# Kernel tuning notes

Hardware: AMD Instinct MI355X
Metric: run time of the kernel (lower is better)

## Reference

```python
import jax, jax.numpy as jnp
import numpy as np

B, L, D_MODEL, D_FF, H = 2, 2048, 512, 512, 8
DK = D_FF // H


def _lin(key, fan_in, fan_out):
    k1, k2 = jax.random.split(key)
    lim = 1.0 / np.sqrt(fan_in)
    W = jax.random.uniform(k1, (fan_in, fan_out), jnp.float32, -lim, lim)
    b = jax.random.uniform(k2, (fan_out,), jnp.float32, -lim, lim)
    return W, b


def setup_inputs() -> dict:
    key = jax.random.key(0)
    ks = jax.random.split(key, 13)
    x = jax.random.normal(ks[0], (B, L, D_MODEL), jnp.float32)
    x_knowledge = jax.random.normal(ks[1], (B, L, D_MODEL), jnp.float32)
    Wv, bv = _lin(ks[2], D_MODEL, D_FF)
    Wk, bk = _lin(ks[3], D_MODEL, D_FF)
    Wq, bq = _lin(ks[4], D_MODEL, D_FF)
    Wkf, bkf = _lin(ks[5], D_MODEL, D_FF)
    Wqf, bqf = _lin(ks[6], D_MODEL, D_FF)
    Wq2, bq2 = _lin(ks[7], D_FF, D_FF)
    Wk2, bk2 = _lin(ks[8], D_FF, D_FF)
    Wkf2, bkf2 = _lin(ks[9], D_FF, D_FF)
    Wqf2, bqf2 = _lin(ks[10], D_FF, D_FF)
    Wo, bo = _lin(ks[11], D_FF, D_MODEL)
    return dict(x=x, x_knowledge=x_knowledge, Wv=Wv, bv=bv, Wk=Wk, bk=bk,
                Wq=Wq, bq=bq, Wkf=Wkf, bkf=bkf, Wqf=Wqf, bqf=bqf,
                Wq2=Wq2, bq2=bq2, Wk2=Wk2, bk2=bk2, Wqf2=Wqf2, bqf2=bqf2,
                Wkf2=Wkf2, bkf2=bkf2, Wo=Wo, bo=bo)


def reference(x, x_knowledge, Wv, bv, Wk, bk, Wq, bq, Wkf, bkf, Wqf, bqf,
              Wq2, bq2, Wk2, bk2, Wqf2, bqf2, Wkf2, bkf2, Wo, bo):
    b, l, _ = x.shape
    # first projections from d_model -> d_ff
    v = x @ Wv + bv
    k = x @ Wk + bk
    q = x @ Wq + bq
    k_fei = x_knowledge @ Wkf + bkf
    q_fei = x_knowledge @ Wqf + bqf
    # second projections + NONSTANDARD head split: raw reshape (B,L,d_ff)->(B,h,L,dk)
    q = (q @ Wq2 + bq2).reshape(b, H, l, DK)
    k = (k @ Wk2 + bk2).reshape(b, H, l, DK)
    q_fei = (q_fei @ Wqf2 + bqf2).reshape(b, H, l, DK)
    k_fei = (k_fei @ Wkf2 + bkf2).reshape(b, H, l, DK)
    scale = 1.0 / np.sqrt(2.0 * DK).astype(np.float32)
    att = jnp.einsum('bhld,bhmd->bhlm', q, k) * scale
    att_fei = jnp.einsum('bhld,bhmd->bhlm', q_fei, k_fei) * scale
    score = jax.nn.softmax(att + att_fei, axis=-1)  # dropout is identity at eval
    v = v.reshape(b, H, l, DK)
    out = jnp.einsum('bhlm,bhmd->bhld', score, v).reshape(b, l, D_FF)
    return out @ Wo + bo
```

## Files before the change

### kernel.cpp

```cpp
#include <hip/hip_runtime.h>
#include <hip/hip_bf16.h>

typedef unsigned short u16;
typedef unsigned int   u32;
typedef __attribute__((ext_vector_type(8))) short bf16x8;
typedef __attribute__((ext_vector_type(4))) float f32x4;

#define SCALE 0.08838834764831845f
#define SCLOG 0.12752040542575836f

__device__ inline u16 f2bf(float f) {
  u32 u = __builtin_bit_cast(u32, f);
  u = (u + 0x7FFFu + ((u >> 16) & 1u)) >> 16;
  return (u16)u;
}
__device__ inline float bf2f(u16 b) {
  u32 u = (u32)b << 16;
  return __builtin_bit_cast(float, u);
}

__global__ __launch_bounds__(256) void cvt_bf16(const float* __restrict__ a,
                                                const float* __restrict__ b,
                                                u16* __restrict__ oa,
                                                u16* __restrict__ ob) {
  const float* in = blockIdx.y ? b : a;
  u16* out = blockIdx.y ? ob : oa;
  const int i = (blockIdx.x * 256 + threadIdx.x) * 8;
  float4 f0 = *(const float4*)(in + i);
  float4 f1 = *(const float4*)(in + i + 4);
  alignas(16) u16 t[8] = {f2bf(f0.x), f2bf(f0.y), f2bf(f0.z), f2bf(f0.w),
                          f2bf(f1.x), f2bf(f1.y), f2bf(f1.z), f2bf(f1.w)};
  *(uint4*)(out + i) = *(const uint4*)t;
}

struct TPtrs { const float* p[10]; };

__global__ __launch_bounds__(256) void transposeW(TPtrs ptrs, u16* __restrict__ out) {
  __shared__ u16 ts[64][65];
  const float sc = (blockIdx.z == 5 || blockIdx.z == 7) ? SCLOG : 1.0f;
  const float* in = ptrs.p[blockIdx.z];
  u16* o = out + (size_t)blockIdx.z * 262144;
  const int t = threadIdx.x;
  const int k0 = blockIdx.y * 64, n0 = blockIdx.x * 64;
  for (int pp = 0; pp < 16; ++pp) {
    int id = t + 256 * pp; int r = id >> 6, c = id & 63;
    ts[r][c] = f2bf(in[(size_t)(k0 + r) * 512 + n0 + c] * sc);
  }
  __syncthreads();
  for (int pp = 0; pp < 16; ++pp) {
    int id = t + 256 * pp; int r = id >> 6, c = id & 63;
    o[(size_t)(n0 + r) * 512 + k0 + c] = ts[c][r];
  }
}

struct BPtrs { const float* p[10]; };

__global__ __launch_bounds__(512) void biasPack(BPtrs bp, float* __restrict__ out) {
  const int z = blockIdx.x, n = threadIdx.x;
  const float sc = (z == 5 || z == 7) ? SCLOG : 1.0f;
  out[z * 512 + n] = bp.p[z][n] * sc;
}

__global__ __launch_bounds__(256) void transposeV(const u16* __restrict__ v1,
                                                  u16* __restrict__ vt) {
  __shared__ u16 ts[64][65];
  const size_t base = (size_t)blockIdx.y * 131072;
  const u16* in = v1 + base;
  u16* out = vt + base;
  const int l0 = blockIdx.x * 64;
  const int t = threadIdx.x;
  const int r = t >> 3, c8 = (t & 7) * 8;
  for (int pp = 0; pp < 2; ++pp) {
    int rr = r + pp * 32;
    *(uint4*)&ts[rr][c8] = *(const uint4*)&in[(size_t)(l0 + rr) * 64 + c8];
  }
  __syncthreads();
  for (int pp = 0; pp < 2; ++pp) {
    int d = r + pp * 32;
    alignas(16) u16 tmp[8];
    #pragma unroll
    for (int i = 0; i < 8; ++i) tmp[i] = ts[c8 + i][d];
    *(uint4*)&out[(size_t)d * 2048 + l0 + c8] = *(const uint4*)tmp;
  }
}

struct GemmBatch {
  const u16* A[4];
  const u16* Ax;
  int xsplit;
  void* out[5];
  int wrow0, zstride;
};

template <typename TOUT>
__global__ __launch_bounds__(256, 2) void gemm3(GemmBatch gb,
    const u16* __restrict__ Wt, const float* __restrict__ biasP) {
  const int tx = blockIdx.x, z = blockIdx.z;
  const u16* A = (tx < gb.xsplit) ? gb.A[z] : gb.Ax;
  const int wrow = gb.wrow0 + z * gb.zstride + tx * 128;
  const int m0 = blockIdx.y * 128;
  const u16* B = Wt + (size_t)wrow * 512;
  const float* bias = biasP + wrow;

  const int t = threadIdx.x, wid = t >> 6, lane = t & 63;
  const int lg = lane >> 4, ln = lane & 15;
  const int wr = wid >> 1, wc = wid & 1;

  __shared__ u16 As[2][128][64];
  __shared__ u16 Bs[2][128][64];

  const int srow = t >> 3, sch = t & 7;
  const int sw = (sch ^ (srow & 7)) * 8;
  const u16* Asrc = A + (size_t)(m0 + srow) * 512 + sch * 8;
  const u16* Bsrc = B + (size_t)srow * 512 + sch * 8;

  uint4 ra[4], rb[4];
  #pragma unroll
  for (int p = 0; p < 4; ++p) {
    ra[p] = *(const uint4*)(Asrc + p * 32 * 512);
    rb[p] = *(const uint4*)(Bsrc + p * 32 * 512);
  }
  #pragma unroll
  for (int p = 0; p < 4; ++p) {
    *(uint4*)&As[0][srow + 32 * p][sw] = ra[p];
    *(uint4*)&Bs[0][srow + 32 * p][sw] = rb[p];
  }
  __syncthreads();

  f32x4 acc[4][4];
  #pragma unroll
  for (int i = 0; i < 4; ++i)
    #pragma unroll
    for (int j = 0; j < 4; ++j)
      #pragma unroll
      for (int r = 0; r < 4; ++r) acc[i][j][r] = 0.0f;

  int cur = 0;
  for (int kt = 0; kt < 8; ++kt) {
    if (kt < 7) {
      const int ko = (kt + 1) * 64;
      #pragma unroll
      for (int p = 0; p < 4; ++p) {
        ra[p] = *(const uint4*)(Asrc + ko + p * 32 * 512);
        rb[p] = *(const uint4*)(Bsrc + ko + p * 32 * 512);
      }
    }
    #pragma unroll
    for (int ck = 0; ck < 2; ++ck) {
      bf16x8 af[4], bfr[4];
      #pragma unroll
      for (int mi = 0; mi < 4; ++mi) {
        const int r = wr * 64 + mi * 16 + ln;
        af[mi] = *(const bf16x8*)&As[cur][r][((ck * 4 + lg) ^ (r & 7)) * 8];
      }
      #pragma unroll
      for (int ni = 0; ni < 4; ++ni) {
        const int r = wc * 64 + ni * 16 + ln;
        bfr[ni] = *(const bf16x8*)&Bs[cur][r][((ck * 4 + lg) ^ (r & 7)) * 8];
      }
      #pragma unroll
      for (int mi = 0; mi < 4; ++mi)
        #pragma unroll
        for (int ni = 0; ni < 4; ++ni)
          acc[mi][ni] = __builtin_amdgcn_mfma_f32_16x16x32_bf16(
              af[mi], bfr[ni], acc[mi][ni], 0, 0, 0);
    }
    if (kt < 7) {
      #pragma unroll
      for (int p = 0; p < 4; ++p) {
        *(uint4*)&As[cur ^ 1][srow + 32 * p][sw] = ra[p];
        *(uint4*)&Bs[cur ^ 1][srow + 32 * p][sw] = rb[p];
      }
      __syncthreads();
      cur ^= 1;
    }
  }

  TOUT* C = (TOUT*)gb.out[(wrow >> 9) - (gb.wrow0 >> 9)];
  const int nbase = wrow & 511;
  #pragma unroll
  for (int ni = 0; ni < 4; ++ni) {
    const int colw = wc * 64 + ni * 16 + ln;
    const float bv = bias[colw];
    const int col = nbase + colw;
    #pragma unroll
    for (int mi = 0; mi < 4; ++mi)
      #pragma unroll
      for (int r = 0; r < 4; ++r) {
        const int row = m0 + wr * 64 + mi * 16 + 4 * lg + r;
        const float val = acc[mi][ni][r] + bv;
        if constexpr (sizeof(TOUT) == 4) C[(size_t)row * 512 + col] = val;
        else                             C[(size_t)row * 512 + col] = f2bf(val);
      }
  }
}

__global__ __launch_bounds__(512) void attn5(
    const u16* __restrict__ q2, const u16* __restrict__ k2,
    const u16* __restrict__ qf2, const u16* __restrict__ kf2,
    const u16* __restrict__ vtg, u16* __restrict__ opart,
    float2* __restrict__ mlbuf) {
  const int id = blockIdx.x;
  const int nid = (id & 7) * 32 + (id >> 3);
  const int split = nid & 1;
  const int qt = (nid >> 1) & 7;
  const int bh = nid >> 4;
  const size_t base = (size_t)bh * 131072;
  const int kv0 = split * 1024;

  const u16* Q  = q2  + base;
  const u16* Qf = qf2 + base;
  u16* Op = opart + (size_t)split * 2097152 + base;

  const int t = threadIdx.x, wid = t >> 6, lane = t & 63;
  const int lg = lane >> 4, ln = lane & 15;
  const int r0 = qt * 256 + wid * 32;

  __shared__ u16 K_s [2][64][64];
  __shared__ u16 Kf_s[2][64][64];
  __shared__ u16 Vt_s[2][64][64];
  __shared__ u16 P_s [8][32][64];

  const int srow = t >> 3, sch = t & 7;
  const int sw = (sch ^ (srow & 7)) * 8;
  const u16* Ksrc  = k2  + base + (size_t)(kv0 + srow) * 64 + sch * 8;
  const u16* Kfsrc = kf2 + base + (size_t)(kv0 + srow) * 64 + sch * 8;
  const u16* Vsrc  = vtg + base + (size_t)srow * 2048 + kv0 + sch * 8;

  bf16x8 aq[2][4];
  #pragma unroll
  for (int mi = 0; mi < 2; ++mi) {
    const int row = r0 + mi * 16 + ln;
    aq[mi][0] = *(const bf16x8*)&Q [row * 64 +      lg * 8];
    aq[mi][1] = *(const bf16x8*)&Q [row * 64 + 32 + lg * 8];
    aq[mi][2] = *(const bf16x8*)&Qf[row * 64 +      lg * 8];
    aq[mi][3] = *(const bf16x8*)&Qf[row * 64 + 32 + lg * 8];
  }

  f32x4 oacc[2][4];
  #pragma unroll
  for (int mi = 0; mi < 2; ++mi)
    #pragma unroll
    for (int df = 0; df < 4; ++df)
      #pragma unroll
      for (int r = 0; r < 4; ++r) oacc[mi][df][r] = 0.0f;
  float m_run[2][4], l_par[2][4];
  #pragma unroll
  for (int mi = 0; mi < 2; ++mi)
    #pragma unroll
    for (int r = 0; r < 4; ++r) { m_run[mi][r] = -1e30f; l_par[mi][r] = 0.0f; }

  uint4 rk = *(const uint4*)(Ksrc);
  uint4 rf = *(const uint4*)(Kfsrc);
  uint4 rv = *(const uint4*)(Vsrc);
  *(uint4*)&K_s [0][srow][sw] = rk;
  *(uint4*)&Kf_s[0][srow][sw] = rf;
  *(uint4*)&Vt_s[0][srow][sw] = rv;
  __syncthreads();

  int cur = 0;
  for (int kt = 0; kt < 16; ++kt) {
    if (kt < 15) {
      const int ko = (kt + 1) * 4096;
      rk = *(const uint4*)(Ksrc  + ko);
      rf = *(const uint4*)(Kfsrc + ko);
      rv = *(const uint4*)(Vsrc  + (kt + 1) * 64);
    }

    f32x4 s[2][4];
    #pragma unroll
    for (int cf = 0; cf < 4; ++cf) {
      const int n = cf * 16 + ln;
      const int sx = n & 7;
      bf16x8 b0 = *(const bf16x8*)&K_s [cur][n][((0 + lg) ^ sx) * 8];
      bf16x8 b1 = *(const bf16x8*)&K_s [cur][n][((4 + lg) ^ sx) * 8];
      bf16x8 b2 = *(const bf16x8*)&Kf_s[cur][n][((0 + lg) ^ sx) * 8];
      bf16x8 b3 = *(const bf16x8*)&Kf_s[cur][n][((4 + lg) ^ sx) * 8];
      #pragma unroll
      for (int mi = 0; mi < 2; ++mi) {
        f32x4 a;
        #pragma unroll
        for (int r = 0; r < 4; ++r) a[r] = 0.0f;
        a = __builtin_amdgcn_mfma_f32_16x16x32_bf16(aq[mi][0], b0, a, 0, 0, 0);
        a = __builtin_amdgcn_mfma_f32_16x16x32_bf16(aq[mi][1], b1, a, 0, 0, 0);
        a = __builtin_amdgcn_mfma_f32_16x16x32_bf16(aq[mi][2], b2, a, 0, 0, 0);
        a = __builtin_amdgcn_mfma_f32_16x16x32_bf16(aq[mi][3], b3, a, 0, 0, 0);
        s[mi][cf] = a;
      }
    }

    float smax[2][4];
    bool viol = false;
    #pragma unroll
    for (int mi = 0; mi < 2; ++mi)
      #pragma unroll
      for (int r = 0; r < 4; ++r) {
        smax[mi][r] = fmaxf(fmaxf(s[mi][0][r], s[mi][1][r]),
                            fmaxf(s[mi][2][r], s[mi][3][r]));
        viol = viol || (smax[mi][r] > m_run[mi][r] + 11.0f);
      }
    if (__any(viol)) {
      #pragma unroll
      for (int off = 1; off < 16; off <<= 1)
        #pragma unroll
        for (int mi = 0; mi < 2; ++mi)
          #pragma unroll
          for (int r = 0; r < 4; ++r)
            smax[mi][r] = fmaxf(smax[mi][r], __shfl_xor(smax[mi][r], off, 64));
      #pragma unroll
      for (int mi = 0; mi < 2; ++mi)
        #pragma unroll
        for (int r = 0; r < 4; ++r) {
          const float mnew = fmaxf(m_run[mi][r], smax[mi][r]);
          const float corr = exp2f(m_run[mi][r] - mnew);
          m_run[mi][r] = mnew;
          l_par[mi][r] *= corr;
          #pragma unroll
          for (int df = 0; df < 4; ++df) oacc[mi][df][r] *= corr;
        }
    }
    #pragma unroll
    for (int mi = 0; mi < 2; ++mi)
      #pragma unroll
      for (int cf = 0; cf < 4; ++cf) {
        const int col = cf * 16 + ln;
        #pragma unroll
        for (int r = 0; r < 4; ++r) {
          const int rr = 4 * lg + r;
          const float p = exp2f(s[mi][cf][r] - m_run[mi][r]);
          l_par[mi][r] += p;
          P_s[wid][mi * 16 + rr][col ^ ((rr & 7) * 8)] =
              __builtin_bit_cast(u16, __float2bfloat16(p));
        }
      }

    #pragma unroll
    for (int kc = 0; kc < 2; ++kc) {
      const int kk = kc * 32 + lg * 8;
      bf16x8 ap0 = *(const bf16x8*)&P_s[wid][ln]     [kk ^ ((ln & 7) * 8)];
      bf16x8 ap1 = *(const bf16x8*)&P_s[wid][16 + ln][kk ^ ((ln & 7) * 8)];
      #pragma unroll
      for (int df = 0; df < 4; ++df) {
        const int n = df * 16 + ln;
        bf16x8 bv = *(const bf16x8*)&Vt_s[cur][n][((kc * 4 + lg) ^ (n & 7)) * 8];
        oacc[0][df] = __builtin_amdgcn_mfma_f32_16x16x32_bf16(ap0, bv, oacc[0][df], 0, 0, 0);
        oacc[1][df] = __builtin_amdgcn_mfma_f32_16x16x32_bf16(ap1, bv, oacc[1][df], 0, 0, 0);
      }
    }

    if (kt < 15) {
      *(uint4*)&K_s [cur ^ 1][srow][sw] = rk;
      *(uint4*)&Kf_s[cur ^ 1][srow][sw] = rf;
      *(uint4*)&Vt_s[cur ^ 1][srow][sw] = rv;
      __syncthreads();
      cur ^= 1;
    }
  }

  #pragma unroll
  for (int off = 1; off < 16; off <<= 1)
    #pragma unroll
    for (int mi = 0; mi < 2; ++mi)
      #pragma unroll
      for (int r = 0; r < 4; ++r)
        l_par[mi][r] += __shfl_xor(l_par[mi][r], off, 64);

  #pragma unroll
  for (int mi = 0; mi < 2; ++mi)
    #pragma unroll
    for (int df = 0; df < 4; ++df)
      #pragma unroll
      for (int r = 0; r < 4; ++r) {
        const int row = r0 + mi * 16 + 4 * lg + r;
        const int col = df * 16 + ln;
        Op[(size_t)row * 64 + col] = f2bf(oacc[mi][df][r]);
      }
  if (ln == 0) {
    #pragma unroll
    for (int mi = 0; mi < 2; ++mi)
      #pragma unroll
      for (int r = 0; r < 4; ++r) {
        const int grow = bh * 2048 + r0 + mi * 16 + 4 * lg + r;
        mlbuf[split * 32768 + grow] = make_float2(m_run[mi][r], l_par[mi][r]);
      }
  }
}

__global__ __launch_bounds__(256) void combine(
    const u16* __restrict__ opart, const float2* __restrict__ mlbuf,
    u16* __restrict__ att) {
  const int gid = blockIdx.x * 256 + threadIdx.x;
  const int row = gid >> 3, c8 = (gid & 7) * 8;
  const float2 ml1 = mlbuf[row];
  const float2 ml2 = mlbuf[32768 + row];
  const float mx = fmaxf(ml1.x, ml2.x);
  const float a1 = exp2f(ml1.x - mx), a2 = exp2f(ml2.x - mx);
  const float inv = 1.0f / (ml1.y * a1 + ml2.y * a2);
  const float w1 = a1 * inv, w2 = a2 * inv;
  uint4 o1 = *(const uint4*)&opart[(size_t)row * 64 + c8];
  uint4 o2 = *(const uint4*)&opart[2097152 + (size_t)row * 64 + c8];
  const u16* p1 = (const u16*)&o1;
  const u16* p2 = (const u16*)&o2;
  alignas(16) u16 ot[8];
  #pragma unroll
  for (int i = 0; i < 8; ++i)
    ot[i] = f2bf(bf2f(p1[i]) * w1 + bf2f(p2[i]) * w2);
  *(uint4*)&att[(size_t)row * 64 + c8] = *(const uint4*)ot;
}

extern "C" void kernel_launch(void* const* d_in, const int* in_sizes, int n_in,
                              void* d_out, int out_size, void* d_ws, size_t ws_size,
                              hipStream_t stream) {
  const float* x    = (const float*)d_in[0];
  const float* xk   = (const float*)d_in[1];
  const float* Wv   = (const float*)d_in[2];  const float* bv   = (const float*)d_in[3];
  const float* Wk   = (const float*)d_in[4];  const float* bk   = (const float*)d_in[5];
  const float* Wq   = (const float*)d_in[6];  const float* bq   = (const float*)d_in[7];
  const float* Wkf  = (const float*)d_in[8];  const float* bkf  = (const float*)d_in[9];
  const float* Wqf  = (const float*)d_in[10]; const float* bqf  = (const float*)d_in[11];
  const float* Wq2  = (const float*)d_in[12]; const float* bq2  = (const float*)d_in[13];
  const float* Wk2  = (const float*)d_in[14]; const float* bk2  = (const float*)d_in[15];
  const float* Wqf2 = (const float*)d_in[16]; const float* bqf2 = (const float*)d_in[17];
  const float* Wkf2 = (const float*)d_in[18]; const float* bkf2 = (const float*)d_in[19];
  const float* Wo   = (const float*)d_in[20]; const float* bo   = (const float*)d_in[21];

  u16* ws = (u16*)d_ws;
  u16* Wt = ws;
  float* biasP = (float*)(ws + 2621440);
  u16* bufs = ws + 2621440 + 10240;
  const size_t BUF = 2097152;
  u16* v1  = bufs + 0 * BUF;
  u16* k1  = bufs + 1 * BUF;
  u16* q1  = bufs + 2 * BUF;
  u16* kf1 = bufs + 3 * BUF;
  u16* qf1 = bufs + 4 * BUF;
  u16* q2  = bufs + 5 * BUF;
  u16* k2  = bufs + 6 * BUF;
  u16* qf2 = bufs + 7 * BUF;
  u16* kf2 = bufs + 8 * BUF;
  float2* mlbuf = (float2*)(bufs + 9 * BUF);

  cvt_bf16<<<dim3(1024, 2), 256, 0, stream>>>(x, xk, q2, k2);

  TPtrs tp;
  tp.p[0] = Wv;  tp.p[1] = Wk;  tp.p[2] = Wq;   tp.p[3] = Wkf;  tp.p[4] = Wqf;
  tp.p[5] = Wq2; tp.p[6] = Wk2; tp.p[7] = Wqf2; tp.p[8] = Wkf2; tp.p[9] = Wo;
  transposeW<<<dim3(8, 8, 10), 256, 0, stream>>>(tp, Wt);

  BPtrs bp;
  bp.p[0] = bv;  bp.p[1] = bk;  bp.p[2] = bq;   bp.p[3] = bkf;  bp.p[4] = bqf;
  bp.p[5] = bq2; bp.p[6] = bk2; bp.p[7] = bqf2; bp.p[8] = bkf2; bp.p[9] = bo;
  biasPack<<<dim3(10), 512, 0, stream>>>(bp, biasP);

  GemmBatch g1 = {};
  g1.A[0] = q2;  g1.Ax = k2;  g1.xsplit = 12;
  g1.out[0] = v1; g1.out[1] = k1; g1.out[2] = q1; g1.out[3] = kf1; g1.out[4] = qf1;
  g1.wrow0 = 0; g1.zstride = 0;
  gemm3<u16><<<dim3(20, 32, 1), 256, 0, stream>>>(g1, Wt, biasP);

  GemmBatch g3 = {};
  g3.A[0] = q1; g3.A[1] = k1; g3.A[2] = qf1; g3.A[3] = kf1;
  g3.Ax = q1; g3.xsplit = 100;
  g3.out[0] = q2; g3.out[1] = k2; g3.out[2] = qf2; g3.out[3] = kf2;
  g3.wrow0 = 2560; g3.zstride = 512;
  gemm3<u16><<<dim3(4, 32, 4), 256, 0, stream>>>(g3, Wt, biasP);

  transposeV<<<dim3(32, 16), 256, 0, stream>>>(v1, q1);

  attn5<<<dim3(256), 512, 0, stream>>>(q2, k2, qf2, kf2, q1, kf1, mlbuf);

  combine<<<dim3(1024), 256, 0, stream>>>(kf1, mlbuf, v1);

  GemmBatch g4 = {};
  g4.A[0] = v1; g4.Ax = v1; g4.xsplit = 100;
  g4.out[0] = d_out;
  g4.wrow0 = 4608; g4.zstride = 0;
  gemm3<float><<<dim3(4, 32, 1), 256, 0, stream>>>(g4, Wt, biasP);
}
```

Baseline: 119.2 us.

## Use direct global-to-LDS loads in GEMM and register-resident P in attention

The GEMM drops register-staged double buffering in favour of single-buffered global_load_lds transfers, halving LDS use so that launch bounds can allow four blocks per CU. The attention kernel computes S transposed (K as the A operand) so each lane holds softmax probabilities that can be packed straight into bf16 MFMA operands. This removes the P shared-memory round trip and its buffer. The row max and sum reductions shrink to two cross-group shuffles, with a new swizzle for the K/V tiles. Risks include losing overlap of loads with compute in the GEMM, since LDS is now unswizzled and single-buffered, and getting the lane mapping of the transposed layout wrong.

New measurement: 117.9 us. Within noise of the previous version (-1.1%).

```diff
diff --git a/kernel.cpp b/kernel.cpp
--- a/kernel.cpp
+++ b/kernel.cpp
@@ -17,6 +17,15 @@
 __device__ inline float bf2f(u16 b) {
   u32 u = (u32)b << 16;
   return __builtin_bit_cast(float, u);
+}
+__device__ inline u32 pkbf(float a, float b) {
+  return (u32)f2bf(a) | ((u32)f2bf(b) << 16);
+}
+
+__device__ __forceinline__ void glds16(const u16* g, u16* l) {
+  __builtin_amdgcn_global_load_lds(
+      (__attribute__((address_space(1))) void*)g,
+      (__attribute__((address_space(3))) void*)l, 16, 0, 0);
 }
 
 __global__ __launch_bounds__(256) void cvt_bf16(const float* __restrict__ a,
@@ -93,7 +102,7 @@
 };
 
 template <typename TOUT>
-__global__ __launch_bounds__(256, 2) void gemm3(GemmBatch gb,
+__global__ __launch_bounds__(256, 4) void gemm4(GemmBatch gb,
     const u16* __restrict__ Wt, const float* __restrict__ biasP) {
   const int tx = blockIdx.x, z = blockIdx.z;
   const u16* A = (tx < gb.xsplit) ? gb.A[z] : gb.Ax;
@@ -106,26 +115,11 @@
   const int lg = lane >> 4, ln = lane & 15;
   const int wr = wid >> 1, wc = wid & 1;
 
-  __shared__ u16 As[2][128][64];
-  __shared__ u16 Bs[2][128][64];
-
-  const int srow = t >> 3, sch = t & 7;
-  const int sw = (sch ^ (srow & 7)) * 8;
-  const u16* Asrc = A + (size_t)(m0 + srow) * 512 + sch * 8;
-  const u16* Bsrc = B + (size_t)srow * 512 + sch * 8;
-
-  uint4 ra[4], rb[4];
-  #pragma unroll
-  for (int p = 0; p < 4; ++p) {
-    ra[p] = *(const uint4*)(Asrc + p * 32 * 512);
-    rb[p] = *(const uint4*)(Bsrc + p * 32 * 512);
-  }
-  #pragma unroll
-  for (int p = 0; p < 4; ++p) {
-    *(uint4*)&As[0][srow + 32 * p][sw] = ra[p];
-    *(uint4*)&Bs[0][srow + 32 * p][sw] = rb[p];
-  }
-  __syncthreads();
+  __shared__ u16 As[128][64];
+  __shared__ u16 Bs[128][64];
+
+  const u16* Ag = A + (size_t)m0 * 512;
+  const int lrow = lane >> 3, lch = lane & 7;
 
   f32x4 acc[4][4];
   #pragma unroll
@@ -135,29 +129,25 @@
       #pragma unroll
       for (int r = 0; r < 4; ++r) acc[i][j][r] = 0.0f;
 
-  int cur = 0;
   for (int kt = 0; kt < 8; ++kt) {
-    if (kt < 7) {
-      const int ko = (kt + 1) * 64;
-      #pragma unroll
-      for (int p = 0; p < 4; ++p) {
-        ra[p] = *(const uint4*)(Asrc + ko + p * 32 * 512);
-        rb[p] = *(const uint4*)(Bsrc + ko + p * 32 * 512);
-      }
-    }
+    #pragma unroll
+    for (int c = 0; c < 4; ++c) {
+      const int row = (wid * 4 + c) * 8 + lrow;
+      const size_t go = (size_t)row * 512 + kt * 64 + lch * 8;
+      glds16(Ag + go, &As[(wid * 4 + c) * 8][0]);
+      glds16(B  + go, &Bs[(wid * 4 + c) * 8][0]);
+    }
+    __syncthreads();
+
     #pragma unroll
     for (int ck = 0; ck < 2; ++ck) {
       bf16x8 af[4], bfr[4];
       #pragma unroll
-      for (int mi = 0; mi < 4; ++mi) {
-        const int r = wr * 64 + mi * 16 + ln;
-        af[mi] = *(const bf16x8*)&As[cur][r][((ck * 4 + lg) ^ (r & 7)) * 8];
-      }
-      #pragma unroll
-      for (int ni = 0; ni < 4; ++ni) {
-        const int r = wc * 64 + ni * 16 + ln;
-        bfr[ni] = *(const bf16x8*)&Bs[cur][r][((ck * 4 + lg) ^ (r & 7)) * 8];
-      }
+      for (int mi = 0; mi < 4; ++mi)
+        af[mi] = *(const bf16x8*)&As[wr * 64 + mi * 16 + ln][ck * 32 + lg * 8];
+      #pragma unroll
+      for (int ni = 0; ni < 4; ++ni)
+        bfr[ni] = *(const bf16x8*)&Bs[wc * 64 + ni * 16 + ln][ck * 32 + lg * 8];
       #pragma unroll
       for (int mi = 0; mi < 4; ++mi)
         #pragma unroll
@@ -165,15 +155,7 @@
           acc[mi][ni] = __builtin_amdgcn_mfma_f32_16x16x32_bf16(
               af[mi], bfr[ni], acc[mi][ni], 0, 0, 0);
     }
-    if (kt < 7) {
-      #pragma unroll
-      for (int p = 0; p < 4; ++p) {
-        *(uint4*)&As[cur ^ 1][srow + 32 * p][sw] = ra[p];
-        *(uint4*)&Bs[cur ^ 1][srow + 32 * p][sw] = rb[p];
-      }
-      __syncthreads();
-      cur ^= 1;
-    }
+    if (kt < 7) __syncthreads();
   }
 
   TOUT* C = (TOUT*)gb.out[(wrow >> 9) - (gb.wrow0 >> 9)];
@@ -195,7 +177,7 @@
   }
 }
 
-__global__ __launch_bounds__(512) void attn5(
+__global__ __launch_bounds__(512) void attn7(
     const u16* __restrict__ q2, const u16* __restrict__ k2,
     const u16* __restrict__ qf2, const u16* __restrict__ kf2,
     const u16* __restrict__ vtg, u16* __restrict__ opart,
@@ -219,36 +201,36 @@
   __shared__ u16 K_s [2][64][64];
   __shared__ u16 Kf_s[2][64][64];
   __shared__ u16 Vt_s[2][64][64];
-  __shared__ u16 P_s [8][32][64];
 
   const int srow = t >> 3, sch = t & 7;
-  const int sw = (sch ^ (srow & 7)) * 8;
+  const int fsr = (srow & 3) | (((srow >> 3) & 1) << 2);
+  const int sw = (sch ^ fsr) * 8;
   const u16* Ksrc  = k2  + base + (size_t)(kv0 + srow) * 64 + sch * 8;
   const u16* Kfsrc = kf2 + base + (size_t)(kv0 + srow) * 64 + sch * 8;
   const u16* Vsrc  = vtg + base + (size_t)srow * 2048 + kv0 + sch * 8;
 
   bf16x8 aq[2][4];
   #pragma unroll
-  for (int mi = 0; mi < 2; ++mi) {
-    const int row = r0 + mi * 16 + ln;
-    aq[mi][0] = *(const bf16x8*)&Q [row * 64 +      lg * 8];
-    aq[mi][1] = *(const bf16x8*)&Q [row * 64 + 32 + lg * 8];
-    aq[mi][2] = *(const bf16x8*)&Qf[row * 64 +      lg * 8];
-    aq[mi][3] = *(const bf16x8*)&Qf[row * 64 + 32 + lg * 8];
+  for (int qb = 0; qb < 2; ++qb) {
+    const int row = r0 + qb * 16 + ln;
+    aq[qb][0] = *(const bf16x8*)&Q [row * 64 +      lg * 8];
+    aq[qb][1] = *(const bf16x8*)&Q [row * 64 + 32 + lg * 8];
+    aq[qb][2] = *(const bf16x8*)&Qf[row * 64 +      lg * 8];
+    aq[qb][3] = *(const bf16x8*)&Qf[row * 64 + 32 + lg * 8];
   }
 
   f32x4 oacc[2][4];
   #pragma unroll
-  for (int mi = 0; mi < 2; ++mi)
+  for (int qb = 0; qb < 2; ++qb)
     #pragma unroll
     for (int df = 0; df < 4; ++df)
       #pragma unroll
-      for (int r = 0; r < 4; ++r) oacc[mi][df][r] = 0.0f;
-  float m_run[2][4], l_par[2][4];
-  #pragma unroll
-  for (int mi = 0; mi < 2; ++mi)
-    #pragma unroll
-    for (int r = 0; r < 4; ++r) { m_run[mi][r] = -1e30f; l_par[mi][r] = 0.0f; }
+      for (int r = 0; r < 4; ++r) oacc[qb][df][r] = 0.0f;
+  float m_run[2], l_par[2];
+  #pragma unroll
+  for (int qb = 0; qb < 2; ++qb) { m_run[qb] = -1e30f; l_par[qb] = 0.0f; }
+
+  const int rbase = 8 * (ln >> 2) + (ln & 3);
 
   uint4 rk = *(const uint4*)(Ksrc);
   uint4 rf = *(const uint4*)(Kfsrc);
@@ -269,84 +251,94 @@
 
     f32x4 s[2][4];
     #pragma unroll
-    for (int cf = 0; cf < 4; ++cf) {
-      const int n = cf * 16 + ln;
-      const int sx = n & 7;
-      bf16x8 b0 = *(const bf16x8*)&K_s [cur][n][((0 + lg) ^ sx) * 8];
-      bf16x8 b1 = *(const bf16x8*)&K_s [cur][n][((4 + lg) ^ sx) * 8];
-      bf16x8 b2 = *(const bf16x8*)&Kf_s[cur][n][((0 + lg) ^ sx) * 8];
-      bf16x8 b3 = *(const bf16x8*)&Kf_s[cur][n][((4 + lg) ^ sx) * 8];
-      #pragma unroll
-      for (int mi = 0; mi < 2; ++mi) {
+    for (int m = 0; m < 4; ++m) {
+      const int rowg = rbase + 4 * (m & 1) + 32 * (m >> 1);
+      const int fz = (rowg & 3) | (((rowg >> 3) & 1) << 2);
+      bf16x8 a0 = *(const bf16x8*)&K_s [cur][rowg][((0 + lg) ^ fz) * 8];
+      bf16x8 a1 = *(const bf16x8*)&K_s [cur][rowg][((4 + lg) ^ fz) * 8];
+      bf16x8 a2 = *(const bf16x8*)&Kf_s[cur][rowg][((0 + lg) ^ fz) * 8];
+      bf16x8 a3 = *(const bf16x8*)&Kf_s[cur][rowg][((4 + lg) ^ fz) * 8];
+      #pragma unroll
+      for (int qb = 0; qb < 2; ++qb) {
         f32x4 a;
         #pragma unroll
         for (int r = 0; r < 4; ++r) a[r] = 0.0f;
-        a = __builtin_amdgcn_mfma_f32_16x16x32_bf16(aq[mi][0], b0, a, 0, 0, 0);
-        a = __builtin_amdgcn_mfma_f32_16x16x32_bf16(aq[mi][1], b1, a, 0, 0, 0);
-        a = __builtin_amdgcn_mfma_f32_16x16x32_bf16(aq[mi][2], b2, a, 0, 0, 0);
-        a = __builtin_amdgcn_mfma_f32_16x16x32_bf16(aq[mi][3], b3, a, 0, 0, 0);
-        s[mi][cf] = a;
-      }
-    }
-
-    float smax[2][4];
+        a = __builtin_amdgcn_mfma_f32_16x16x32_bf16(a0, aq[qb][0], a, 0, 0, 0);
+        a = __builtin_amdgcn_mfma_f32_16x16x32_bf16(a1, aq[qb][1], a, 0, 0, 0);
+        a = __builtin_amdgcn_mfma_f32_16x16x32_bf16(a2, aq[qb][2], a, 0, 0, 0);
+        a = __builtin_amdgcn_mfma_f32_16x16x32_bf16(a3, aq[qb][3], a, 0, 0, 0);
+        s[qb][m] = a;
+      }
+    }
+
+    float smax[2];
     bool viol = false;
     #pragma unroll
-    for (int mi = 0; mi < 2; ++mi)
-      #pragma unroll
-      for (int r = 0; r < 4; ++r) {
-        smax[mi][r] = fmaxf(fmaxf(s[mi][0][r], s[mi][1][r]),
-                            fmaxf(s[mi][2][r], s[mi][3][r]));
-        viol = viol || (smax[mi][r] > m_run[mi][r] + 11.0f);
-      }
+    for (int qb = 0; qb < 2; ++qb) {
+      float v = fmaxf(fmaxf(s[qb][0][0], s[qb][0][1]),
+                      fmaxf(s[qb][0][2], s[qb][0][3]));
+      #pragma unroll
+      for (int m = 1; m < 4; ++m)
+        v = fmaxf(v, fmaxf(fmaxf(s[qb][m][0], s[qb][m][1]),
+                           fmaxf(s[qb][m][2], s[qb][m][3])));
+      smax[qb] = v;
+      viol = viol || (v > m_run[qb] + 11.0f);
+    }
     if (__any(viol)) {
-      #pragma unroll
-      for (int off = 1; off < 16; off <<= 1)
-        #pragma unroll
-        for (int mi = 0; mi < 2; ++mi)
-          #pragma unroll
-          for (int r = 0; r < 4; ++r)
-            smax[mi][r] = fmaxf(smax[mi][r], __shfl_xor(smax[mi][r], off, 64));
-      #pragma unroll
-      for (int mi = 0; mi < 2; ++mi)
+      float corrq[2];
+      #pragma unroll
+      for (int qb = 0; qb < 2; ++qb) {
+        float v = smax[qb];
+        v = fmaxf(v, __shfl_xor(v, 16, 64));
+        v = fmaxf(v, __shfl_xor(v, 32, 64));
+        const float mnew = fmaxf(m_run[qb], v);
+        corrq[qb] = exp2f(m_run[qb] - mnew);
+        m_run[qb] = mnew;
+        l_par[qb] *= corrq[qb];
+      }
+      #pragma unroll
+      for (int qb = 0; qb < 2; ++qb)
         #pragma unroll
         for (int r = 0; r < 4; ++r) {
-          const float mnew = fmaxf(m_run[mi][r], smax[mi][r]);
-          const float corr = exp2f(m_run[mi][r] - mnew);
-          m_run[mi][r] = mnew;
-          l_par[mi][r] *= corr;
+          const float c = __shfl(corrq[qb], 4 * lg + r, 64);
           #pragma unroll
-          for (int df = 0; df < 4; ++df) oacc[mi][df][r] *= corr;
+          for (int df = 0; df < 4; ++df) oacc[qb][df][r] *= c;
         }
     }
-    #pragma unroll
-    for (int mi = 0; mi < 2; ++mi)
-      #pragma unroll
-      for (int cf = 0; cf < 4; ++cf) {
-        const int col = cf * 16 + ln;
+
+    bf16x8 pa[2][2];
+    #pragma unroll
+    for (int qb = 0; qb < 2; ++qb) {
+      float pf[4][4];
+      #pragma unroll
+      for (int m = 0; m < 4; ++m)
         #pragma unroll
         for (int r = 0; r < 4; ++r) {
-          const int rr = 4 * lg + r;
-          const float p = exp2f(s[mi][cf][r] - m_run[mi][r]);
-          l_par[mi][r] += p;
-          P_s[wid][mi * 16 + rr][col ^ ((rr & 7) * 8)] =
-              __builtin_bit_cast(u16, __float2bfloat16(p));
+          const float p = exp2f(s[qb][m][r] - m_run[qb]);
+          l_par[qb] += p;
+          pf[m][r] = p;
         }
-      }
-
-    #pragma unroll
-    for (int kc = 0; kc < 2; ++kc) {
-      const int kk = kc * 32 + lg * 8;
-      bf16x8 ap0 = *(const bf16x8*)&P_s[wid][ln]     [kk ^ ((ln & 7) * 8)];
-      bf16x8 ap1 = *(const bf16x8*)&P_s[wid][16 + ln][kk ^ ((ln & 7) * 8)];
+      #pragma unroll
+      for (int kc = 0; kc < 2; ++kc) {
+        union { u32 w[4]; bf16x8 v; } U;
+        U.w[0] = pkbf(pf[2 * kc][0],     pf[2 * kc][1]);
+        U.w[1] = pkbf(pf[2 * kc][2],     pf[2 * kc][3]);
+        U.w[2] = pkbf(pf[2 * kc + 1][0], pf[2 * kc + 1][1]);
+        U.w[3] = pkbf(pf[2 * kc + 1][2], pf[2 * kc + 1][3]);
+        pa[qb][kc] = U.v;
+      }
+    }
+
+    #pragma unroll
+    for (int kc = 0; kc < 2; ++kc)
       #pragma unroll
       for (int df = 0; df < 4; ++df) {
-        const int n = df * 16 + ln;
-        bf16x8 bv = *(const bf16x8*)&Vt_s[cur][n][((kc * 4 + lg) ^ (n & 7)) * 8];
-        oacc[0][df] = __builtin_amdgcn_mfma_f32_16x16x32_bf16(ap0, bv, oacc[0][df], 0, 0, 0);
-        oacc[1][df] = __builtin_amdgcn_mfma_f32_16x16x32_bf16(ap1, bv, oacc[1][df], 0, 0, 0);
-      }
-    }
+        const int rv = 16 * df + ln;
+        const int fz = (rv & 3) | (((rv >> 3) & 1) << 2);
+        bf16x8 bv = *(const bf16x8*)&Vt_s[cur][rv][((kc * 4 + lg) ^ fz) * 8];
+        oacc[0][df] = __builtin_amdgcn_mfma_f32_16x16x32_bf16(pa[0][kc], bv, oacc[0][df], 0, 0, 0);
+        oacc[1][df] = __builtin_amdgcn_mfma_f32_16x16x32_bf16(pa[1][kc], bv, oacc[1][df], 0, 0, 0);
+      }
 
     if (kt < 15) {
       *(uint4*)&K_s [cur ^ 1][srow][sw] = rk;
@@ -358,31 +350,27 @@
   }
 
   #pragma unroll
-  for (int off = 1; off < 16; off <<= 1)
-    #pragma unroll
-    for (int mi = 0; mi < 2; ++mi)
-      #pragma unroll
-      for (int r = 0; r < 4; ++r)
-        l_par[mi][r] += __shfl_xor(l_par[mi][r], off, 64);
-
-  #pragma unroll
-  for (int mi = 0; mi < 2; ++mi)
+  for (int qb = 0; qb < 2; ++qb) {
+    l_par[qb] += __shfl_xor(l_par[qb], 16, 64);
+    l_par[qb] += __shfl_xor(l_par[qb], 32, 64);
+  }
+
+  #pragma unroll
+  for (int qb = 0; qb < 2; ++qb)
     #pragma unroll
     for (int df = 0; df < 4; ++df)
       #pragma unroll
       for (int r = 0; r < 4; ++r) {
-        const int row = r0 + mi * 16 + 4 * lg + r;
+        const int row = r0 + qb * 16 + 4 * lg + r;
         const int col = df * 16 + ln;
-        Op[(size_t)row * 64 + col] = f2bf(oacc[mi][df][r]);
-      }
-  if (ln == 0) {
-    #pragma unroll
-    for (int mi = 0; mi < 2; ++mi)
-      #pragma unroll
-      for (int r = 0; r < 4; ++r) {
-        const int grow = bh * 2048 + r0 + mi * 16 + 4 * lg + r;
-        mlbuf[split * 32768 + grow] = make_float2(m_run[mi][r], l_par[mi][r]);
-      }
+        Op[(size_t)row * 64 + col] = f2bf(oacc[qb][df][r]);
+      }
+  if (lane < 16) {
+    #pragma unroll
+    for (int qb = 0; qb < 2; ++qb) {
+      const int grow = bh * 2048 + r0 + qb * 16 + ln;
+      mlbuf[split * 32768 + grow] = make_float2(m_run[qb], l_par[qb]);
+    }
   }
 }
 
@@ -456,18 +444,18 @@
   g1.A[0] = q2;  g1.Ax = k2;  g1.xsplit = 12;
   g1.out[0] = v1; g1.out[1] = k1; g1.out[2] = q1; g1.out[3] = kf1; g1.out[4] = qf1;
   g1.wrow0 = 0; g1.zstride = 0;
-  gemm3<u16><<<dim3(20, 32, 1), 256, 0, stream>>>(g1, Wt, biasP);
+  gemm4<u16><<<dim3(20, 32, 1), 256, 0, stream>>>(g1, Wt, biasP);
 
   GemmBatch g3 = {};
   g3.A[0] = q1; g3.A[1] = k1; g3.A[2] = qf1; g3.A[3] = kf1;
   g3.Ax = q1; g3.xsplit = 100;
   g3.out[0] = q2; g3.out[1] = k2; g3.out[2] = qf2; g3.out[3] = kf2;
   g3.wrow0 = 2560; g3.zstride = 512;
-  gemm3<u16><<<dim3(4, 32, 4), 256, 0, stream>>>(g3, Wt, biasP);
+  gemm4<u16><<<dim3(4, 32, 4), 256, 0, stream>>>(g3, Wt, biasP);
 
   transposeV<<<dim3(32, 16), 256, 0, stream>>>(v1, q1);
 
-  attn5<<<dim3(256), 512, 0, stream>>>(q2, k2, qf2, kf2, q1, kf1, mlbuf);
+  attn7<<<dim3(256), 512, 0, stream>>>(q2, k2, qf2, kf2, q1, kf1, mlbuf);
 
   combine<<<dim3(1024), 256, 0, stream>>>(kf1, mlbuf, v1);
 
@@ -475,5 +463,5 @@
   g4.A[0] = v1; g4.Ax = v1; g4.xsplit = 100;
   g4.out[0] = d_out;
   g4.wrow0 = 4608; g4.zstride = 0;
-  gemm3<float><<<dim3(4, 32, 1), 256, 0, stream>>>(g4, Wt, biasP);
-}
+  gemm4<float><<<dim3(4, 32, 1), 256, 0, stream>>>(g4, Wt, biasP);
+}
```
